# Kernel optimization log

Measured on AMD Instinct MI355X. Metric: run time of the kernel, lower is better.

## Reference

```python
import jax, jax.numpy as jnp
import numpy as np

N_NODES = 50000
N_EDGES = 800000
IN_CH = 16
HIDDEN = [128, 128, 128]
OUT_CH = 16
SELF_LOOP_W = 2.0  # improved=True


def _glorot(key, fan_in, fan_out):
    s = jnp.sqrt(6.0 / (fan_in + fan_out))
    return jax.random.uniform(key, (fan_in, fan_out), jnp.float32, -s, s)


def setup_inputs() -> dict:
    key = jax.random.key(0)
    ks = jax.random.split(key, 12)
    x = jax.random.normal(ks[0], (N_NODES, IN_CH), jnp.float32)
    edge_index = jax.random.randint(ks[1], (2, N_EDGES), 0, N_NODES, jnp.int64)
    edge_attr = jax.random.uniform(ks[2], (N_EDGES,), jnp.float32)
    dims = [IN_CH] + HIDDEN + [OUT_CH]
    inp = {"x": x, "edge_index": edge_index, "edge_attr": edge_attr}
    for i in range(4):
        inp[f"w{i}"] = _glorot(ks[3 + i], dims[i], dims[i + 1])
        inp[f"b{i}"] = jnp.zeros((dims[i + 1],), jnp.float32)
    return inp


def _gcn_norm(edge_index, edge_attr, n):
    # add self-loops with weight 2.0 (improved=True), symmetric normalization
    src = jnp.concatenate([edge_index[0], jnp.arange(n, dtype=edge_index.dtype)])
    dst = jnp.concatenate([edge_index[1], jnp.arange(n, dtype=edge_index.dtype)])
    w = jnp.concatenate([edge_attr, jnp.full((n,), SELF_LOOP_W, edge_attr.dtype)])
    deg = jax.ops.segment_sum(w, dst, num_segments=n)
    dinv = jnp.where(deg > 0, jax.lax.rsqrt(jnp.where(deg > 0, deg, 1.0)), 0.0)
    norm = dinv[src] * w * dinv[dst]
    return src, dst, norm


def _gcn_conv(x, src, dst, norm, w, b, n):
    h = x @ w                                   # [N, out]
    msg = norm[:, None] * h[src]                # gather + scale, [E+N, out]
    return jax.ops.segment_sum(msg, dst, num_segments=n) + b


def reference(x, edge_index, edge_attr, w0, b0, w1, b1, w2, b2, w3, b3):
    n = x.shape[0]
    src, dst, norm = _gcn_norm(edge_index, edge_attr, n)
    ws = [(w0, b0), (w1, b1), (w2, b2), (w3, b3)]
    for i, (w, b) in enumerate(ws):
        x = _gcn_conv(x, src, dst, norm, w, b, n)
        if i < len(ws) - 1:
            x = jax.nn.relu(x)
    return x
```

## Files before the change

kernel.cpp:

```cpp
#include <hip/hip_runtime.h>
#include <hip/hip_fp16.h>


static constexpr int NN = 50000;
static constexpr int NE = 800000;
static constexpr int ROW_U = 80;

typedef _Float16 half8_t __attribute__((ext_vector_type(8)));
typedef float float4_t __attribute__((ext_vector_type(4)));

union Frag { uint4 u; half8_t h; };
union H2U2 { uint2 u; __half2 h[2]; };
union H4U4 { uint4 u; __half2 h[4]; };

__device__ __forceinline__ float unpack_w(uint e) {
  return __half2float(__ushort_as_half((ushort)(e >> 16)));
}


__global__ void prep_kernel(const float* __restrict__ w1, const float* __restrict__ w2,
                            const float* __restrict__ w3, char* __restrict__ wt1,
                            char* __restrict__ wt2, char* __restrict__ wt3,
                            uint* __restrict__ csr) {
  int t = blockIdx.x * blockDim.x + threadIdx.x;
  if (t < NN) csr[(size_t)t * ROW_U] = 0u;
  if (t < 16384) {
    int k = t >> 7, n = t & 127;
    int off = n * 256 + ((2 * k) ^ ((n & 7) << 4));
    *(ushort*)(wt1 + off) = __half_as_ushort(__float2half(w1[t]));
    *(ushort*)(wt2 + off) = __half_as_ushort(__float2half(w2[t]));
  }
  if (t < 2048) {
    int k = t >> 4, n = t & 15;
    *(ushort*)(wt3 + n * 256 + ((2 * k) ^ ((n & 7) << 4))) = __half_as_ushort(__float2half(w3[t]));
  }
}

__global__ void fill_pad_kernel(const int* __restrict__ src, const int* __restrict__ dst,
                                const float* __restrict__ ea, uint* __restrict__ csr, int ne) {
  int i = blockIdx.x * blockDim.x + threadIdx.x;
  if (i < ne) {
    int d = dst[i];
    uint packed = ((uint)__half_as_ushort(__float2half(ea[i])) << 16) | (uint)src[i];
    int slot = atomicAdd((int*)(csr + (size_t)d * ROW_U), 1);
    csr[(size_t)d * ROW_U + 4 + slot] = packed;
  }
}

__global__ void row_deg_xscale_kernel(const uint* __restrict__ csr, const float* __restrict__ x,
                                      float* __restrict__ dinv, __half* __restrict__ xs, int n) {
  int i = blockIdx.x * blockDim.x + threadIdx.x;
  if (i >= n) return;
  const uint* row = csr + (size_t)i * ROW_U;
  const int cn = (int)row[0];
  float d = 2.0f;
  int e = 0;
  for (; e + 4 <= cn; e += 4) {
    uint4 q = *(const uint4*)(row + 4 + e);
    d += unpack_w(q.x) + unpack_w(q.y) + unpack_w(q.z) + unpack_w(q.w);
  }
  for (; e < cn; ++e) d += unpack_w(row[4 + e]);
  float dn = rsqrtf(d);
  dinv[i] = dn;
  const float4* xr = (const float4*)(x + (size_t)i * 16);
  uint2* xo = (uint2*)(xs + (size_t)i * 16);
#pragma unroll
  for (int q = 0; q < 4; ++q) {
    float4 v = xr[q];
    H2U2 pk;
    pk.h[0] = __float22half2_rn(make_float2(dn * v.x, dn * v.y));
    pk.h[1] = __float22half2_rn(make_float2(dn * v.z, dn * v.w));
    xo[q] = pk.u;
  }
}


template <bool FINAL>
__global__ void __launch_bounds__(256) gather16_kernel(
    const __half* __restrict__ g, const uint* __restrict__ csr, const float* __restrict__ dinv,
    const float* __restrict__ bias, void* __restrict__ dest, int n) {
  const int node = blockIdx.x * 64 + (threadIdx.x >> 2);
  const int cg = threadIdx.x & 3;
  if (node >= n) return;
  const uint2* g2 = (const uint2*)g;
  H2U2 self; self.u = g2[(size_t)node * 4 + cg];
  float2 s0 = __half22float2(self.h[0]), s1 = __half22float2(self.h[1]);
  float4 acc = make_float4(2.f * s0.x, 2.f * s0.y, 2.f * s1.x, 2.f * s1.y);

  const uint* row = csr + (size_t)node * ROW_U;
  const int cn = (int)row[0];
  int e = 0;
  for (; e + 4 <= cn; e += 4) {
    uint4 q = *(const uint4*)(row + 4 + e);
    uint ev[4] = {q.x, q.y, q.z, q.w};
    H2U2 v[4];
#pragma unroll
    for (int j = 0; j < 4; ++j) v[j].u = g2[(size_t)(ev[j] & 0xFFFFu) * 4 + cg];
#pragma unroll
    for (int j = 0; j < 4; ++j) {
      float w = unpack_w(ev[j]);
      float2 f0 = __half22float2(v[j].h[0]), f1 = __half22float2(v[j].h[1]);
      acc.x = fmaf(w, f0.x, acc.x); acc.y = fmaf(w, f0.y, acc.y);
      acc.z = fmaf(w, f1.x, acc.z); acc.w = fmaf(w, f1.y, acc.w);
    }
  }
  for (; e < cn; ++e) {
    uint ev = row[4 + e];
    H2U2 v; v.u = g2[(size_t)(ev & 0xFFFFu) * 4 + cg];
    float w = unpack_w(ev);
    float2 f0 = __half22float2(v.h[0]), f1 = __half22float2(v.h[1]);
    acc.x = fmaf(w, f0.x, acc.x); acc.y = fmaf(w, f0.y, acc.y);
    acc.z = fmaf(w, f1.x, acc.z); acc.w = fmaf(w, f1.y, acc.w);
  }
  float dn = dinv[node];
  if (FINAL) {
    float4 bv = ((const float4*)bias)[cg];
    ((float4*)dest)[(size_t)node * 4 + cg] =
        make_float4(dn * acc.x + bv.x, dn * acc.y + bv.y, dn * acc.z + bv.z, dn * acc.w + bv.w);
  } else {
    H2U2 pk;
    pk.h[0] = __float22half2_rn(make_float2(dn * acc.x, dn * acc.y));
    pk.h[1] = __float22half2_rn(make_float2(dn * acc.z, dn * acc.w));
    ((uint2*)dest)[(size_t)node * 4 + cg] = pk.u;
  }
}

__global__ void __launch_bounds__(256) gather128_kernel(
    const __half* __restrict__ g, const uint* __restrict__ csr, const float* __restrict__ dinv,
    const float* __restrict__ bias, __half* __restrict__ aggh, int n) {
  const int node = blockIdx.x * 16 + (threadIdx.x >> 4);
  const int cg = threadIdx.x & 15;
  if (node >= n) return;
  const uint4* g4 = (const uint4*)g;
  float acc[8];
  {
    H4U4 self; self.u = g4[(size_t)node * 16 + cg];
    float2 f0 = __half22float2(self.h[0]), f1 = __half22float2(self.h[1]);
    float2 f2 = __half22float2(self.h[2]), f3 = __half22float2(self.h[3]);
    acc[0] = 2.f * f0.x; acc[1] = 2.f * f0.y; acc[2] = 2.f * f1.x; acc[3] = 2.f * f1.y;
    acc[4] = 2.f * f2.x; acc[5] = 2.f * f2.y; acc[6] = 2.f * f3.x; acc[7] = 2.f * f3.y;
  }
  const uint* row = csr + (size_t)node * ROW_U;
  const int cn = (int)row[0];
  int e = 0;
  for (; e + 4 <= cn; e += 4) {
    uint4 q = *(const uint4*)(row + 4 + e);
    uint ev[4] = {q.x, q.y, q.z, q.w};
    H4U4 v[4];
#pragma unroll
    for (int j = 0; j < 4; ++j) v[j].u = g4[(size_t)(ev[j] & 0xFFFFu) * 16 + cg];
#pragma unroll
    for (int j = 0; j < 4; ++j) {
      float w = unpack_w(ev[j]);
      float2 f0 = __half22float2(v[j].h[0]), f1 = __half22float2(v[j].h[1]);
      float2 f2 = __half22float2(v[j].h[2]), f3 = __half22float2(v[j].h[3]);
      acc[0] = fmaf(w, f0.x, acc[0]); acc[1] = fmaf(w, f0.y, acc[1]);
      acc[2] = fmaf(w, f1.x, acc[2]); acc[3] = fmaf(w, f1.y, acc[3]);
      acc[4] = fmaf(w, f2.x, acc[4]); acc[5] = fmaf(w, f2.y, acc[5]);
      acc[6] = fmaf(w, f3.x, acc[6]); acc[7] = fmaf(w, f3.y, acc[7]);
    }
  }
  for (; e < cn; ++e) {
    uint ev = row[4 + e];
    H4U4 v; v.u = g4[(size_t)(ev & 0xFFFFu) * 16 + cg];
    float w = unpack_w(ev);
    float2 f0 = __half22float2(v.h[0]), f1 = __half22float2(v.h[1]);
    float2 f2 = __half22float2(v.h[2]), f3 = __half22float2(v.h[3]);
    acc[0] = fmaf(w, f0.x, acc[0]); acc[1] = fmaf(w, f0.y, acc[1]);
    acc[2] = fmaf(w, f1.x, acc[2]); acc[3] = fmaf(w, f1.y, acc[3]);
    acc[4] = fmaf(w, f2.x, acc[4]); acc[5] = fmaf(w, f2.y, acc[5]);
    acc[6] = fmaf(w, f3.x, acc[6]); acc[7] = fmaf(w, f3.y, acc[7]);
  }
  const float dn = dinv[node];
  const float4* b4 = (const float4*)bias;
  float4 bl = b4[cg * 2], bh = b4[cg * 2 + 1];
  float r[8];
  r[0] = fmaxf(dn * acc[0] + bl.x, 0.f); r[1] = fmaxf(dn * acc[1] + bl.y, 0.f);
  r[2] = fmaxf(dn * acc[2] + bl.z, 0.f); r[3] = fmaxf(dn * acc[3] + bl.w, 0.f);
  r[4] = fmaxf(dn * acc[4] + bh.x, 0.f); r[5] = fmaxf(dn * acc[5] + bh.y, 0.f);
  r[6] = fmaxf(dn * acc[6] + bh.z, 0.f); r[7] = fmaxf(dn * acc[7] + bh.w, 0.f);
  H4U4 pk;
  pk.h[0] = __float22half2_rn(make_float2(r[0], r[1]));
  pk.h[1] = __float22half2_rn(make_float2(r[2], r[3]));
  pk.h[2] = __float22half2_rn(make_float2(r[4], r[5]));
  pk.h[3] = __float22half2_rn(make_float2(r[6], r[7]));
  ((uint4*)aggh)[(size_t)node * 16 + cg] = pk.u;
}


__global__ void __launch_bounds__(256) mfma128x128_kernel(
    const __half* __restrict__ Ah, const char* __restrict__ wt,
    const float* __restrict__ dinv, __half* __restrict__ outg, int n) {
  __shared__ char wts[32768];
  for (int i = threadIdx.x; i < 2048; i += 256)
    ((uint4*)wts)[i] = ((const uint4*)wt)[i];
  __syncthreads();
  const int row0 = blockIdx.x * 64;
  const int wave = threadIdx.x >> 6, lane = threadIdx.x & 63;
  const int lr = lane & 15, hi = lane >> 4;
  const int rowL = wave * 16 + lr;
  const char* Arow = (const char*)(Ah + (size_t)(row0 + rowL) * 128);
  const int sw = (lr & 7) << 4;
  float4_t acc[8];
#pragma unroll
  for (int ct = 0; ct < 8; ++ct) acc[ct] = (float4_t){0.f, 0.f, 0.f, 0.f};
#pragma unroll
  for (int k0 = 0; k0 < 128; k0 += 32) {
    const int kb = 2 * k0 + hi * 8;
    uint2 alo = *(const uint2*)(Arow + kb);
    uint2 ahi2 = *(const uint2*)(Arow + kb + 32);
    Frag a; a.u = make_uint4(alo.x, alo.y, ahi2.x, ahi2.y);
#pragma unroll
    for (int ct = 0; ct < 8; ++ct) {
      const char* brow = wts + (ct * 16 + lr) * 256;
      uint2 blo = *(const uint2*)(brow + (kb ^ sw));
      uint2 bhi2 = *(const uint2*)(brow + ((kb + 32) ^ sw));
      Frag b; b.u = make_uint4(blo.x, blo.y, bhi2.x, bhi2.y);
      acc[ct] = __builtin_amdgcn_mfma_f32_16x16x32_f16(a.h, b.h, acc[ct], 0, 0, 0);
    }
  }
  int rr[4]; float dnv[4];
#pragma unroll
  for (int reg = 0; reg < 4; ++reg) {
    rr[reg] = row0 + wave * 16 + hi * 4 + reg;
    dnv[reg] = (rr[reg] < n) ? dinv[rr[reg]] : 0.f;
  }
#pragma unroll
  for (int ct = 0; ct < 8; ++ct) {
    int c = ct * 16 + lr;
#pragma unroll
    for (int reg = 0; reg < 4; ++reg)
      if (rr[reg] < n)
        outg[(size_t)rr[reg] * 128 + c] = __float2half(dnv[reg] * acc[ct][reg]);
  }
}

__global__ void __launch_bounds__(256) mfma128x16_kernel(
    const __half* __restrict__ Ah, const char* __restrict__ wt,
    const float* __restrict__ dinv, __half* __restrict__ outg, int n) {
  __shared__ char wts[4096];
  if (threadIdx.x < 256) ((uint4*)wts)[threadIdx.x] = ((const uint4*)wt)[threadIdx.x];
  __syncthreads();
  const int row0 = blockIdx.x * 64;
  const int wave = threadIdx.x >> 6, lane = threadIdx.x & 63;
  const int lr = lane & 15, hi = lane >> 4;
  const int rowL = wave * 16 + lr;
  const char* Arow = (const char*)(Ah + (size_t)(row0 + rowL) * 128);
  const int sw = (lr & 7) << 4;
  const char* brow = wts + lr * 256;
  float4_t acc = (float4_t){0.f, 0.f, 0.f, 0.f};
#pragma unroll
  for (int k0 = 0; k0 < 128; k0 += 32) {
    const int kb = 2 * k0 + hi * 8;
    uint2 alo = *(const uint2*)(Arow + kb);
    uint2 ahi2 = *(const uint2*)(Arow + kb + 32);
    Frag a; a.u = make_uint4(alo.x, alo.y, ahi2.x, ahi2.y);
    uint2 blo = *(const uint2*)(brow + (kb ^ sw));
    uint2 bhi2 = *(const uint2*)(brow + ((kb + 32) ^ sw));
    Frag b; b.u = make_uint4(blo.x, blo.y, bhi2.x, bhi2.y);
    acc = __builtin_amdgcn_mfma_f32_16x16x32_f16(a.h, b.h, acc, 0, 0, 0);
  }
#pragma unroll
  for (int reg = 0; reg < 4; ++reg) {
    int r = row0 + wave * 16 + hi * 4 + reg;
    if (r < n) outg[(size_t)r * 16 + lr] = __float2half(dinv[r] * acc[reg]);
  }
}

__global__ void __launch_bounds__(256) fused_l0l1_kernel(
    const __half* __restrict__ A16h, const float* __restrict__ w0, const float* __restrict__ b0,
    const char* __restrict__ wt1, const float* __restrict__ dinv, __half* __restrict__ g1, int n) {
  __shared__ float a0[64][17];
  __shared__ float ws0[16 * 128];
  __shared__ float bs0[128];
  __shared__ char wts[32768];
  __shared__ char x1s[16384];
  const int row0 = blockIdx.x * 64;
  for (int i = threadIdx.x; i < 2048; i += 256)
    ((uint4*)wts)[i] = ((const uint4*)wt1)[i];
  for (int i = threadIdx.x; i < 512; i += 256)
    ((float4*)ws0)[i] = ((const float4*)w0)[i];
  if (threadIdx.x < 128) bs0[threadIdx.x] = b0[threadIdx.x];
  {
    int r = threadIdx.x >> 2, c8 = threadIdx.x & 3;
    H2U2 v; v.u = make_uint2(0u, 0u);
    if (row0 + r < n) v.u = ((const uint2*)(A16h + (size_t)(row0 + r) * 16))[c8];
    float2 f0 = __half22float2(v.h[0]), f1 = __half22float2(v.h[1]);
    a0[r][c8 * 4 + 0] = f0.x; a0[r][c8 * 4 + 1] = f0.y;
    a0[r][c8 * 4 + 2] = f1.x; a0[r][c8 * 4 + 3] = f1.y;
  }
  __syncthreads();

  {
    const int rg = threadIdx.x >> 4;
    const int c0 = (threadIdx.x & 15) << 3;
    float acc1[4][8];
#pragma unroll
    for (int i = 0; i < 4; ++i)
#pragma unroll
      for (int j = 0; j < 8; ++j) acc1[i][j] = bs0[c0 + j];
#pragma unroll
    for (int k = 0; k < 16; ++k) {
      float A0 = a0[rg * 4 + 0][k], A1 = a0[rg * 4 + 1][k];
      float A2 = a0[rg * 4 + 2][k], A3 = a0[rg * 4 + 3][k];
#pragma unroll
      for (int j = 0; j < 8; ++j) {
        float b = ws0[k * 128 + c0 + j];
        acc1[0][j] = fmaf(A0, b, acc1[0][j]);
        acc1[1][j] = fmaf(A1, b, acc1[1][j]);
        acc1[2][j] = fmaf(A2, b, acc1[2][j]);
        acc1[3][j] = fmaf(A3, b, acc1[3][j]);
      }
    }
#pragma unroll
    for (int i = 0; i < 4; ++i) {
      int row = rg * 4 + i;
      int swz = (row & 7) << 4;
#pragma unroll
      for (int jp = 0; jp < 4; ++jp) {
        int j = jp * 2;
        __half2 h = __float22half2_rn(make_float2(fmaxf(acc1[i][j], 0.f), fmaxf(acc1[i][j + 1], 0.f)));
        *(uint*)(x1s + row * 256 + ((2 * (c0 + j)) ^ swz)) = *(uint*)&h;
      }
    }
  }
  __syncthreads();

  const int wave = threadIdx.x >> 6, lane = threadIdx.x & 63;
  const int lr = lane & 15, hi = lane >> 4;
  const int rowL = wave * 16 + lr;
  const char* Arow = x1s + rowL * 256;
  const int swa = (rowL & 7) << 4;
  const int swb = (lr & 7) << 4;
  float4_t acc[8];
#pragma unroll
  for (int ct = 0; ct < 8; ++ct) acc[ct] = (float4_t){0.f, 0.f, 0.f, 0.f};
#pragma unroll
  for (int k0 = 0; k0 < 128; k0 += 32) {
    const int kb = 2 * k0 + hi * 8;
    uint2 alo = *(const uint2*)(Arow + (kb ^ swa));
    uint2 ahi2 = *(const uint2*)(Arow + ((kb + 32) ^ swa));
    Frag a; a.u = make_uint4(alo.x, alo.y, ahi2.x, ahi2.y);
#pragma unroll
    for (int ct = 0; ct < 8; ++ct) {
      const char* brow = wts + (ct * 16 + lr) * 256;
      uint2 blo = *(const uint2*)(brow + (kb ^ swb));
      uint2 bhi2 = *(const uint2*)(brow + ((kb + 32) ^ swb));
      Frag b; b.u = make_uint4(blo.x, blo.y, bhi2.x, bhi2.y);
      acc[ct] = __builtin_amdgcn_mfma_f32_16x16x32_f16(a.h, b.h, acc[ct], 0, 0, 0);
    }
  }
  int rr[4]; float dnv[4];
#pragma unroll
  for (int reg = 0; reg < 4; ++reg) {
    rr[reg] = row0 + wave * 16 + hi * 4 + reg;
    dnv[reg] = (rr[reg] < n) ? dinv[rr[reg]] : 0.f;
  }
#pragma unroll
  for (int ct = 0; ct < 8; ++ct) {
    int c = ct * 16 + lr;
#pragma unroll
    for (int reg = 0; reg < 4; ++reg)
      if (rr[reg] < n)
        g1[(size_t)rr[reg] * 128 + c] = __float2half(dnv[reg] * acc[ct][reg]);
  }
}


extern "C" void kernel_launch(void* const* d_in, const int* in_sizes, int n_in,
                              void* d_out, int out_size, void* d_ws, size_t ws_size,
                              hipStream_t stream) {
  const float* x  = (const float*)d_in[0];
  const int*   ei = (const int*)d_in[1];
  const float* ea = (const float*)d_in[2];
  const float* w0 = (const float*)d_in[3];
  const float* b0 = (const float*)d_in[4];
  const float* w1 = (const float*)d_in[5];
  const float* b1 = (const float*)d_in[6];
  const float* w2 = (const float*)d_in[7];
  const float* b2 = (const float*)d_in[8];
  const float* w3 = (const float*)d_in[9];
  const float* b3 = (const float*)d_in[10];
  float* out = (float*)d_out;

  const int* src = ei;
  const int* dst = ei + NE;

  __half* Ah   = (__half*)d_ws;
  __half* gbuf = Ah + (size_t)NN * 128;
  float*  dinv = (float*)(gbuf + (size_t)NN * 128);
  char*   wt1  = (char*)(dinv + ((NN + 63) & ~63));
  char*   wt2  = wt1 + 32768;
  char*   wt3  = wt2 + 32768;
  uint*   csr  = (uint*)(wt3 + 4096);

  const int B = 256;
  auto blocks = [](long long t) { return (int)((t + 255) / 256); };
  const int gb64 = (NN + 63) / 64;

  prep_kernel<<<blocks(NN), B, 0, stream>>>(w1, w2, w3, wt1, wt2, wt3, csr);
  fill_pad_kernel<<<blocks(NE), B, 0, stream>>>(src, dst, ea, csr, NE);
  row_deg_xscale_kernel<<<blocks(NN), B, 0, stream>>>(csr, x, dinv, gbuf, NN);

  gather16_kernel<false><<<(NN + 63) / 64, B, 0, stream>>>(gbuf, csr, dinv, nullptr, Ah, NN);
  fused_l0l1_kernel<<<gb64, B, 0, stream>>>(Ah, w0, b0, wt1, dinv, gbuf, NN);

  gather128_kernel<<<(NN + 15) / 16, B, 0, stream>>>(gbuf, csr, dinv, b1, Ah, NN);
  mfma128x128_kernel<<<gb64, B, 0, stream>>>(Ah, wt2, dinv, gbuf, NN);

  gather128_kernel<<<(NN + 15) / 16, B, 0, stream>>>(gbuf, csr, dinv, b2, Ah, NN);
  mfma128x16_kernel<<<gb64, B, 0, stream>>>(Ah, wt3, dinv, gbuf, NN);

  gather16_kernel<true><<<(NN + 63) / 64, B, 0, stream>>>(gbuf, csr, dinv, b3, out, NN);
}
```

Measured before the change: 185.1 us.

## Build padded CSR via bucketed counting sort instead of global atomics

```diff
diff --git a/kernel.cpp b/kernel.cpp
--- a/kernel.cpp
+++ b/kernel.cpp
@@ -5,6 +5,10 @@
 static constexpr int NN = 50000;
 static constexpr int NE = 800000;
 static constexpr int ROW_U = 80;
+static constexpr int NBKT = (NN + 63) / 64;
+static constexpr int BCAP = 1280;
+static constexpr int EPB = 4096;
+static constexpr int NBLK = (NE + EPB - 1) / EPB;
 
 typedef _Float16 half8_t __attribute__((ext_vector_type(8)));
 typedef float float4_t __attribute__((ext_vector_type(4)));
@@ -20,10 +24,8 @@
 
 __global__ void prep_kernel(const float* __restrict__ w1, const float* __restrict__ w2,
                             const float* __restrict__ w3, char* __restrict__ wt1,
-                            char* __restrict__ wt2, char* __restrict__ wt3,
-                            uint* __restrict__ csr) {
+                            char* __restrict__ wt2, char* __restrict__ wt3) {
   int t = blockIdx.x * blockDim.x + threadIdx.x;
-  if (t < NN) csr[(size_t)t * ROW_U] = 0u;
   if (t < 16384) {
     int k = t >> 7, n = t & 127;
     int off = n * 256 + ((2 * k) ^ ((n & 7) << 4));
@@ -36,41 +38,99 @@
   }
 }
 
-__global__ void fill_pad_kernel(const int* __restrict__ src, const int* __restrict__ dst,
-                                const float* __restrict__ ea, uint* __restrict__ csr, int ne) {
-  int i = blockIdx.x * blockDim.x + threadIdx.x;
-  if (i < ne) {
-    int d = dst[i];
-    uint packed = ((uint)__half_as_ushort(__float2half(ea[i])) << 16) | (uint)src[i];
-    int slot = atomicAdd((int*)(csr + (size_t)d * ROW_U), 1);
-    csr[(size_t)d * ROW_U + 4 + slot] = packed;
-  }
-}
-
-__global__ void row_deg_xscale_kernel(const uint* __restrict__ csr, const float* __restrict__ x,
-                                      float* __restrict__ dinv, __half* __restrict__ xs, int n) {
-  int i = blockIdx.x * blockDim.x + threadIdx.x;
-  if (i >= n) return;
-  const uint* row = csr + (size_t)i * ROW_U;
-  const int cn = (int)row[0];
-  float d = 2.0f;
-  int e = 0;
-  for (; e + 4 <= cn; e += 4) {
-    uint4 q = *(const uint4*)(row + 4 + e);
-    d += unpack_w(q.x) + unpack_w(q.y) + unpack_w(q.z) + unpack_w(q.w);
-  }
-  for (; e < cn; ++e) d += unpack_w(row[4 + e]);
-  float dn = rsqrtf(d);
-  dinv[i] = dn;
-  const float4* xr = (const float4*)(x + (size_t)i * 16);
-  uint2* xo = (uint2*)(xs + (size_t)i * 16);
-#pragma unroll
-  for (int q = 0; q < 4; ++q) {
-    float4 v = xr[q];
-    H2U2 pk;
-    pk.h[0] = __float22half2_rn(make_float2(dn * v.x, dn * v.y));
-    pk.h[1] = __float22half2_rn(make_float2(dn * v.z, dn * v.w));
-    xo[q] = pk.u;
+__global__ void __launch_bounds__(256) hist_kernel(const int* __restrict__ dst,
+                                                   int* __restrict__ blockhist, int ne) {
+  __shared__ int bin[NBKT];
+  const int b = blockIdx.x, t = threadIdx.x;
+  for (int k = t; k < NBKT; k += 256) bin[k] = 0;
+  __syncthreads();
+  const int e0 = b * EPB, e1 = min(e0 + EPB, ne);
+  for (int i = e0 + t; i < e1; i += 256) atomicAdd(&bin[dst[i] >> 6], 1);
+  __syncthreads();
+  for (int k = t; k < NBKT; k += 256) blockhist[(size_t)k * NBLK + b] = bin[k];
+}
+
+__global__ void __launch_bounds__(256) bscan_kernel(int* __restrict__ blockhist,
+                                                    int* __restrict__ bucket_total) {
+  __shared__ int s[256];
+  const int bkt = blockIdx.x, t = threadIdx.x;
+  int v = (t < NBLK) ? blockhist[(size_t)bkt * NBLK + t] : 0;
+  s[t] = v;
+  __syncthreads();
+  for (int off = 1; off < 256; off <<= 1) {
+    int u = (t >= off) ? s[t - off] : 0;
+    __syncthreads();
+    s[t] += u;
+    __syncthreads();
+  }
+  if (t < NBLK) blockhist[(size_t)bkt * NBLK + t] = s[t] - v;
+  if (t == 255) bucket_total[bkt] = s[255];
+}
+
+__global__ void __launch_bounds__(256) scat_kernel(
+    const int* __restrict__ src, const int* __restrict__ dst, const float* __restrict__ ea,
+    const int* __restrict__ blockbase, uint2* __restrict__ sorted, int ne) {
+  __shared__ int lbase[NBKT];
+  __shared__ int lbin[NBKT];
+  const int b = blockIdx.x, t = threadIdx.x;
+  for (int k = t; k < NBKT; k += 256) {
+    lbase[k] = blockbase[(size_t)k * NBLK + b];
+    lbin[k] = 0;
+  }
+  __syncthreads();
+  const int e0 = b * EPB, e1 = min(e0 + EPB, ne);
+  for (int i = e0 + t; i < e1; i += 256) {
+    const int d = dst[i];
+    const int bkt = d >> 6;
+    const int r = atomicAdd(&lbin[bkt], 1);
+    const uint entry = ((uint)__half_as_ushort(__float2half(ea[i])) << 16) | (uint)src[i];
+    sorted[(size_t)bkt * BCAP + lbase[bkt] + r] = make_uint2((uint)d, entry);
+  }
+}
+
+__global__ void __launch_bounds__(256) build_kernel(
+    const uint2* __restrict__ sorted, const int* __restrict__ bucket_total,
+    const float* __restrict__ x, uint* __restrict__ csr, float* __restrict__ dinv,
+    __half* __restrict__ xs, int n) {
+  __shared__ int lcnt[64], lpos[64];
+  __shared__ float ldeg[64], ldinv[64];
+  const int bkt = blockIdx.x, t = threadIdx.x;
+  if (t < 64) { lcnt[t] = 0; lpos[t] = 0; ldeg[t] = 0.f; }
+  __syncthreads();
+  const int d0 = bkt * 64;
+  const int cn = bucket_total[bkt];
+  const uint2* base = sorted + (size_t)bkt * BCAP;
+  for (int i = t; i < cn; i += 256) {
+    uint2 e = base[i];
+    int ld = (int)e.x - d0;
+    atomicAdd(&lcnt[ld], 1);
+    atomicAdd(&ldeg[ld], unpack_w(e.y));
+  }
+  __syncthreads();
+  if (t < 64 && d0 + t < n) {
+    csr[(size_t)(d0 + t) * ROW_U] = (uint)lcnt[t];
+    float dn = rsqrtf(2.f + ldeg[t]);
+    ldinv[t] = dn;
+    dinv[d0 + t] = dn;
+  }
+  __syncthreads();
+  for (int i = t; i < cn; i += 256) {
+    uint2 e = base[i];
+    int ld = (int)e.x - d0;
+    int slot = atomicAdd(&lpos[ld], 1);
+    csr[(size_t)e.x * ROW_U + 4 + slot] = e.y;
+  }
+  {
+    const int nd = t >> 2, c4 = t & 3;
+    const int node = d0 + nd;
+    if (node < n) {
+      float dn = ldinv[nd];
+      float4 v = ((const float4*)(x + (size_t)node * 16))[c4];
+      H2U2 pk;
+      pk.h[0] = __float22half2_rn(make_float2(dn * v.x, dn * v.y));
+      pk.h[1] = __float22half2_rn(make_float2(dn * v.z, dn * v.w));
+      ((uint2*)(xs + (size_t)node * 16))[c4] = pk.u;
+    }
   }
 }
 
@@ -386,21 +446,25 @@
   const int* src = ei;
   const int* dst = ei + NE;
 
-  __half* Ah   = (__half*)d_ws;
-  __half* gbuf = Ah + (size_t)NN * 128;
-  float*  dinv = (float*)(gbuf + (size_t)NN * 128);
-  char*   wt1  = (char*)(dinv + ((NN + 63) & ~63));
-  char*   wt2  = wt1 + 32768;
-  char*   wt3  = wt2 + 32768;
-  uint*   csr  = (uint*)(wt3 + 4096);
+  __half* Ah    = (__half*)d_ws;
+  __half* gbuf  = Ah + (size_t)NN * 128;
+  float*  dinv  = (float*)(gbuf + (size_t)NN * 128);
+  char*   wt1   = (char*)(dinv + ((NN + 63) & ~63));
+  char*   wt2   = wt1 + 32768;
+  char*   wt3   = wt2 + 32768;
+  uint*   csr   = (uint*)(wt3 + 4096);
+  uint2*  sorted = (uint2*)(csr + (size_t)NN * ROW_U);
+  int*    blockhist = (int*)(sorted + (size_t)NBKT * BCAP);
+  int*    bucket_total = blockhist + ((NBKT * NBLK + 15) & ~15);
 
   const int B = 256;
-  auto blocks = [](long long t) { return (int)((t + 255) / 256); };
   const int gb64 = (NN + 63) / 64;
 
-  prep_kernel<<<blocks(NN), B, 0, stream>>>(w1, w2, w3, wt1, wt2, wt3, csr);
-  fill_pad_kernel<<<blocks(NE), B, 0, stream>>>(src, dst, ea, csr, NE);
-  row_deg_xscale_kernel<<<blocks(NN), B, 0, stream>>>(csr, x, dinv, gbuf, NN);
+  prep_kernel<<<64, B, 0, stream>>>(w1, w2, w3, wt1, wt2, wt3);
+  hist_kernel<<<NBLK, B, 0, stream>>>(dst, blockhist, NE);
+  bscan_kernel<<<NBKT, B, 0, stream>>>(blockhist, bucket_total);
+  scat_kernel<<<NBLK, B, 0, stream>>>(src, dst, ea, blockhist, sorted, NE);
+  build_kernel<<<NBKT, B, 0, stream>>>(sorted, bucket_total, x, csr, dinv, gbuf, NN);
 
   gather16_kernel<false><<<(NN + 63) / 64, B, 0, stream>>>(gbuf, csr, dinv, nullptr, Ah, NN);
   fused_l0l1_kernel<<<gb64, B, 0, stream>>>(Ah, w0, b0, wt1, dinv, gbuf, NN);
```

Result: faster. 173.8 us (-6.1%).
